# Performance work log

Measured on AMD Instinct MI355X. Metric: run time of the kernel, lower is better.

Reference implementation:

```python
import jax, jax.numpy as jnp
import numpy as np

N_P = 100000
N_A = 100000
IN = 128
H = 4
D = 32
E = 500000
ALPHA = 0.2


def _leaky(x, a=ALPHA):
    return jnp.where(x > 0, x, a * x)


def _gat_relation(Wh_src_rel, Wh_dst_self, a_src, a_dst, src, dst, n_dst):
    # Wh_src_rel: [Ns,H,D] relation-transformed source feats
    # Wh_dst_self: [Nd,H,D] self-transformed dest feats
    # a_src, a_dst: [H,D] attention vectors; src/dst: [E] edge index
    es = jnp.einsum('nhd,hd->nh', Wh_src_rel, a_src)  # [Ns,H]
    ed = jnp.einsum('nhd,hd->nh', Wh_dst_self, a_dst)  # [Nd,H]
    e = _leaky(es[src] + ed[dst])                      # [E,H]
    m = jax.ops.segment_max(e, dst, num_segments=n_dst)
    m = jnp.where(jnp.isfinite(m), m, 0.0)             # empty segments
    m = jax.lax.stop_gradient(m)
    ee = jnp.exp(e - m[dst])
    s = jax.ops.segment_sum(ee, dst, num_segments=n_dst)
    a = ee / s[dst]                                    # edge_softmax [E,H]
    msg = Wh_src_rel[src] * a[:, :, None]              # [E,H,D]
    return jax.ops.segment_sum(msg, dst, num_segments=n_dst)  # [Nd,H,D]


def setup_inputs() -> dict:
    key = jax.random.key(0)
    ks = jax.random.split(key, 32)
    inp = {
        'feat_P': jax.random.normal(ks[0], (N_P, IN), jnp.float32),
        'feat_A': jax.random.normal(ks[1], (N_A, IN), jnp.float32),
    }
    names = ['p2p', 'p2a', 'a2p', 'a2a']
    nsrc = {'p2p': N_P, 'p2a': N_P, 'a2p': N_A, 'a2a': N_A}
    ndst = {'p2p': N_P, 'p2a': N_A, 'a2p': N_P, 'a2a': N_A}
    for i, r in enumerate(names):
        inp['src_' + r] = jax.random.randint(ks[2 + 2 * i], (E,), 0, nsrc[r], jnp.int32)
        inp['dst_' + r] = jax.random.randint(ks[3 + 2 * i], (E,), 0, ndst[r], jnp.int32)
    # linear weights (torch Linear: y = x @ W.T + b); store as [IN, H*D]
    sc = 1.0 / np.sqrt(IN)
    for i, nm in enumerate(['P', 'A', 'p2p', 'p2a', 'a2p', 'a2a']):
        inp['W_' + nm] = jax.random.uniform(ks[10 + i], (IN, H * D), jnp.float32, -sc, sc)
        inp['b_' + nm] = jax.random.uniform(ks[16 + i], (H * D,), jnp.float32, -sc, sc)
    # attention vectors [H,D]
    for i, nm in enumerate(['p2p_src', 'p2p_dst', 'p2a_src', 'p2a_dst',
                            'a2p_src', 'a2p_dst', 'a2a_src', 'a2a_dst']):
        inp['att_' + nm] = jax.random.normal(ks[22 + i], (H, D), jnp.float32) * 0.1
    return inp


def reference(feat_P, feat_A,
              src_p2p, dst_p2p, src_p2a, dst_p2a,
              src_a2p, dst_a2p, src_a2a, dst_a2a,
              W_P, b_P, W_A, b_A, W_p2p, b_p2p, W_p2a, b_p2a,
              W_a2p, b_a2p, W_a2a, b_a2a,
              att_p2p_src, att_p2p_dst, att_p2a_src, att_p2a_dst,
              att_a2p_src, att_a2p_dst, att_a2a_src, att_a2a_dst):
    lin = lambda x, W, b: (x @ W + b).reshape(-1, H, D)
    Whp = lin(feat_P, W_P, b_P)      # [N_P,H,D]
    Wha = lin(feat_A, W_A, b_A)      # [N_A,H,D]
    Whp2p = lin(feat_P, W_p2p, b_p2p)
    Whp2a = lin(feat_P, W_p2a, b_p2a)
    Wha2p = lin(feat_A, W_a2p, b_a2p)
    Wha2a = lin(feat_A, W_a2a, b_a2a)
    ft_p2p = _gat_relation(Whp2p, Whp, att_p2p_src, att_p2p_dst, src_p2p, dst_p2p, N_P)
    ft_p2a = _gat_relation(Whp2a, Wha, att_p2a_src, att_p2a_dst, src_p2a, dst_p2a, N_A)
    ft_a2p = _gat_relation(Wha2p, Whp, att_a2p_src, att_a2p_dst, src_a2p, dst_a2p, N_P)
    ft_a2a = _gat_relation(Wha2a, Wha, att_a2a_src, att_a2a_dst, src_a2a, dst_a2a, N_A)
    h_P = jax.nn.relu(Whp + ft_p2p + ft_a2p)
    h_A = jax.nn.relu(Wha + ft_p2a + ft_a2a)
    return h_P, h_A
```

## Files before the change

### kernel.cpp

```cpp
#include <hip/hip_runtime.h>
#include <float.h>

#define ALPHA 0.2f
__device__ __forceinline__ float leakyf(float x) { return x > 0.0f ? x : ALPHA * x; }

__device__ __forceinline__ unsigned short f2bf(float f) {
    unsigned u = __float_as_uint(f);
    return (unsigned short)((u + 0x7FFFu + ((u >> 16) & 1u)) >> 16);
}
__device__ __forceinline__ float bflo(unsigned u) { return __uint_as_float(u << 16); }
__device__ __forceinline__ float bfhi(unsigned u) { return __uint_as_float(u & 0xFFFF0000u); }

typedef short bf16x8 __attribute__((ext_vector_type(8)));
typedef float f32x4 __attribute__((ext_vector_type(4)));

struct Ptr4i { const int* p0; const int* p1; const int* p2; const int* p3; };
struct PrepM { const float* W; const float* b; const float* attA; const float* attB; };

__global__ __launch_bounds__(256) void prep_kernel(
    PrepM m0, PrepM m1, PrepM m2, PrepM m3, PrepM m4, PrepM m5,
    bf16x8* __restrict__ wfrag, float* __restrict__ cd,
    int* __restrict__ bcnt, int nz)
{
    int mi = blockIdx.x;
    PrepM mm = (mi == 0) ? m0 : (mi == 1) ? m1 : (mi == 2) ? m2 :
               (mi == 3) ? m3 : (mi == 4) ? m4 : m5;
    int part = blockIdx.y;
    if (mi == 0 && part == 0) {
        for (int i = threadIdx.x; i < nz; i += 256) bcnt[i] = 0;
    }
    for (int ii = 0; ii < 3; ++ii) {
        int c = part * 576 + threadIdx.x + 256 * ii;
        if (c >= part * 576 + 576) continue;
        int t = c >> 8;
        int kstep = (c >> 6) & 3;
        int l = c & 63;
        int k0 = kstep * 32 + (l >> 4) * 8;
        bf16x8 out;
        if (t < 8) {
            int col = t * 16 + (l & 15);
            #pragma unroll
            for (int j = 0; j < 8; ++j)
                out[j] = (short)f2bf(mm.W[(size_t)(k0 + j) * 128 + col]);
        } else {
            int cl = l & 15;
            const float* att = nullptr; int h = 0;
            if (cl < 4 && mm.attA) { att = mm.attA; h = cl; }
            else if (cl >= 4 && cl < 8 && mm.attB) { att = mm.attB; h = cl - 4; }
            #pragma unroll
            for (int j = 0; j < 8; ++j) {
                float s = 0.f;
                if (att) {
                    const float* wrow = mm.W + (size_t)(k0 + j) * 128 + h * 32;
                    for (int d = 0; d < 32; ++d) s += wrow[d] * att[h * 32 + d];
                }
                out[j] = (short)f2bf(s);
            }
        }
        wfrag[(size_t)mi * 2304 + c] = out;
    }
    if (part == 0 && threadIdx.x < 8) {
        int cl = threadIdx.x;
        float s = 0.f;
        const float* att = nullptr; int h = 0;
        if (cl < 4 && mm.attA) { att = mm.attA; h = cl; }
        else if (cl >= 4 && mm.attB) { att = mm.attB; h = cl - 4; }
        if (att) for (int d = 0; d < 32; ++d) s += mm.b[h * 32 + d] * att[h * 32 + d];
        cd[mi * 8 + cl] = s;
    }
}

__device__ __forceinline__ void mfma_compute_store(
    const short* xs_s, const short* wl_s, int row0, int N,
    const float* __restrict__ b, float* __restrict__ o32, unsigned short* __restrict__ o16,
    float* __restrict__ dotA, float* __restrict__ dotB, const float* __restrict__ cd)
{
    int l = threadIdx.x & 63, w = threadIdx.x >> 6;
    int cl = l & 15, gq = l >> 4;
    f32x4 acc[9];
    #pragma unroll
    for (int t = 0; t < 9; ++t) acc[t] = (f32x4){0.f, 0.f, 0.f, 0.f};
    int arow = w * 16 + cl;
    #pragma unroll
    for (int ks = 0; ks < 4; ++ks) {
        int k8 = ks * 4 + gq;
        bf16x8 a = *(const bf16x8*)((const char*)xs_s + arow * 256 + ((k8 * 16) ^ ((arow & 7) << 4)));
        #pragma unroll
        for (int t = 0; t < 9; ++t) {
            bf16x8 bf = *(const bf16x8*)((const char*)wl_s + ((t * 4 + ks) * 64 + l) * 16);
            acc[t] = __builtin_amdgcn_mfma_f32_16x16x32_bf16(a, bf, acc[t], 0, 0, 0);
        }
    }
    int rbase = row0 + w * 16 + gq * 4;
    #pragma unroll
    for (int t = 0; t < 8; ++t) {
        int col = t * 16 + cl;
        float bias = b[col];
        #pragma unroll
        for (int j = 0; j < 4; ++j) {
            int row = rbase + j;
            if (row < N) {
                float v = acc[t][j] + bias;
                if (o32) o32[(size_t)row * 128 + col] = v;
                else     o16[(size_t)row * 128 + col] = f2bf(v);
            }
        }
    }
    if (cl < 8) {
        float cdv = cd[cl];
        float* dp = (cl < 4) ? dotA : dotB;
        int h = cl & 3;
        if (dp) {
            #pragma unroll
            for (int j = 0; j < 4; ++j) {
                int row = rbase + j;
                if (row < N) dp[(size_t)row * 4 + h] = acc[8][j] + cdv;
            }
        }
    }
}

struct Lin3Cfg {
    const float* x; int N; int blocks;
    const bf16x8* wfrag; const float* cd;
    const float* b0; float* o0; float* dA0; float* dB0;
    const float* b1; unsigned short* o1; float* dA1;
    const float* b2; unsigned short* o2; float* dA2;
};

__global__ __launch_bounds__(256) void lin3_mfma_kernel(Lin3Cfg cP, Lin3Cfg cA)
{
    __shared__ short xs_s[64 * 128];
    __shared__ short wl_s[2304 * 8];
    const bool isP = blockIdx.x < (unsigned)cP.blocks;
    const Lin3Cfg& c = isP ? cP : cA;
    const int bx = isP ? blockIdx.x : (blockIdx.x - cP.blocks);
    const int row0 = bx * 64;
    const int N = c.N;

    #pragma unroll
    for (int ii = 0; ii < 4; ++ii) {
        int ci = threadIdx.x + 256 * ii;
        int r = ci >> 4, k8 = ci & 15;
        int srcrow = row0 + r; if (srcrow >= N) srcrow = N - 1;
        const float4* gp = (const float4*)(c.x + (size_t)srcrow * 128 + k8 * 8);
        float4 v0 = gp[0], v1 = gp[1];
        bf16x8 p;
        p[0] = (short)f2bf(v0.x); p[1] = (short)f2bf(v0.y);
        p[2] = (short)f2bf(v0.z); p[3] = (short)f2bf(v0.w);
        p[4] = (short)f2bf(v1.x); p[5] = (short)f2bf(v1.y);
        p[6] = (short)f2bf(v1.z); p[7] = (short)f2bf(v1.w);
        *(bf16x8*)((char*)xs_s + r * 256 + ((k8 * 16) ^ ((r & 7) << 4))) = p;
    }
    #pragma unroll
    for (int ii = 0; ii < 9; ++ii)
        ((bf16x8*)wl_s)[threadIdx.x + 256 * ii] = c.wfrag[threadIdx.x + 256 * ii];
    __syncthreads();
    mfma_compute_store(xs_s, wl_s, row0, N, c.b0, c.o0, nullptr, c.dA0, c.dB0, c.cd);

    __syncthreads();
    #pragma unroll
    for (int ii = 0; ii < 9; ++ii)
        ((bf16x8*)wl_s)[threadIdx.x + 256 * ii] = c.wfrag[2304 + threadIdx.x + 256 * ii];
    __syncthreads();
    mfma_compute_store(xs_s, wl_s, row0, N, c.b1, nullptr, c.o1, c.dA1, nullptr, c.cd + 8);

    __syncthreads();
    #pragma unroll
    for (int ii = 0; ii < 9; ++ii)
        ((bf16x8*)wl_s)[threadIdx.x + 256 * ii] = c.wfrag[2 * 2304 + threadIdx.x + 256 * ii];
    __syncthreads();
    mfma_compute_store(xs_s, wl_s, row0, N, c.b2, nullptr, c.o2, c.dA2, nullptr, c.cd + 16);
}


__global__ __launch_bounds__(256) void binA_count_kernel(Ptr4i dsts, int* __restrict__ bcnt,
                                                         int nbkMax, int E)
{
    __shared__ int lh[4][128];
    ((int*)lh)[threadIdx.x] = 0;
    ((int*)lh)[threadIdx.x + 256] = 0;
    __syncthreads();
    int r = blockIdx.y;
    int w = threadIdx.x >> 6;
    const int* dst = (r == 0) ? dsts.p0 : (r == 1) ? dsts.p1 : (r == 2) ? dsts.p2 : dsts.p3;
    int base = blockIdx.x * 4096;
    #pragma unroll 4
    for (int ii = 0; ii < 16; ++ii) {
        int i = base + threadIdx.x + 256 * ii;
        if (i < E) atomicAdd(&lh[w][dst[i] >> 10], 1);
    }
    __syncthreads();
    if (threadIdx.x < 128) {
        int v = lh[0][threadIdx.x] + lh[1][threadIdx.x] + lh[2][threadIdx.x] + lh[3][threadIdx.x];
        if (v && threadIdx.x < nbkMax) atomicAdd(&bcnt[r * nbkMax + threadIdx.x], v);
    }
}

__global__ __launch_bounds__(512) void bin_scan_kernel(const int* __restrict__ bcnt,
                                                       int* __restrict__ bbase,
                                                       int* __restrict__ gwptr, int nbkMax)
{
    __shared__ int sh[4][128];
    int r = threadIdx.x >> 7, b = threadIdx.x & 127;
    int v = (b < nbkMax) ? bcnt[r * nbkMax + b] : 0;
    sh[r][b] = v;
    __syncthreads();
    #pragma unroll
    for (int off = 1; off < 128; off <<= 1) {
        int y = (b >= off) ? sh[r][b - off] : 0;
        __syncthreads();
        sh[r][b] += y;
        __syncthreads();
    }
    if (b < nbkMax) {
        int ex = sh[r][b] - v;
        bbase[r * nbkMax + b] = ex;
        gwptr[r * nbkMax + b] = ex;
    }
}

__global__ __launch_bounds__(256) void binA_scatter_kernel(Ptr4i dsts, Ptr4i srcs,
    int* __restrict__ gwptr, unsigned* __restrict__ packed, int nbkMax, int E)
{
    __shared__ int lh[128], loff[128], lptr[128], gb[128];
    __shared__ unsigned stg[4096];
    __shared__ unsigned short sb[4096];
    if (threadIdx.x < 128) lh[threadIdx.x] = 0;
    __syncthreads();
    int r = blockIdx.y;
    const int* dst = (r == 0) ? dsts.p0 : (r == 1) ? dsts.p1 : (r == 2) ? dsts.p2 : dsts.p3;
    const int* src = (r == 0) ? srcs.p0 : (r == 1) ? srcs.p1 : (r == 2) ? srcs.p2 : srcs.p3;
    int base = blockIdx.x * 4096;
    int d16[16], s16[16];
    #pragma unroll 4
    for (int ii = 0; ii < 16; ++ii) {
        int i = base + threadIdx.x + 256 * ii;
        if (i < E) {
            d16[ii] = dst[i];
            s16[ii] = src[i];
            atomicAdd(&lh[d16[ii] >> 10], 1);
        } else d16[ii] = -1;
    }
    __syncthreads();
    if (threadIdx.x == 0) {
        int run = 0;
        for (int b = 0; b < nbkMax; ++b) { loff[b] = run; lptr[b] = run; run += lh[b]; }
    }
    __syncthreads();
    #pragma unroll 4
    for (int ii = 0; ii < 16; ++ii) {
        if (d16[ii] >= 0) {
            int b = d16[ii] >> 10;
            int p = atomicAdd(&lptr[b], 1);
            stg[p] = ((unsigned)s16[ii] << 10) | (unsigned)(d16[ii] & 1023);
            sb[p] = (unsigned short)b;
        }
    }
    __syncthreads();
    if (threadIdx.x < nbkMax && lh[threadIdx.x])
        gb[threadIdx.x] = atomicAdd(&gwptr[r * nbkMax + threadIdx.x], lh[threadIdx.x]);
    __syncthreads();
    int tot = min(4096, E - base);
    #pragma unroll 4
    for (int ii = 0; ii < 16; ++ii) {
        int p = threadIdx.x + 256 * ii;
        if (p < tot) {
            int b = sb[p];
            packed[(size_t)r * E + gb[b] + (p - loff[b])] = stg[p];
        }
    }
}

__global__ __launch_bounds__(256) void binB_build_kernel(
    const unsigned* __restrict__ packed, const int* __restrict__ bcnt, const int* __restrict__ bbase,
    int nbkMax, int4 Ns, int E, int stride,
    int* __restrict__ start, int* __restrict__ deg, int* __restrict__ csrc)
{
    int r = blockIdx.y, b = blockIdx.x;
    int N = (r == 0) ? Ns.x : (r == 1) ? Ns.y : (r == 2) ? Ns.z : Ns.w;
    int dst0 = b << 10;
    if (dst0 >= N) return;
    int cnt  = bcnt[r * nbkMax + b];
    int base = bbase[r * nbkMax + b];
    __shared__ int hist[1024];
    __shared__ int sums[256];
    #pragma unroll
    for (int i = 0; i < 4; ++i) hist[threadIdx.x * 4 + i] = 0;
    __syncthreads();
    const unsigned* pk = packed + (size_t)r * E + base;
    for (int i = threadIdx.x; i < cnt; i += 256)
        atomicAdd(&hist[pk[i] & 1023], 1);
    __syncthreads();
    int v4[4], s = 0;
    #pragma unroll
    for (int i = 0; i < 4; ++i) { v4[i] = hist[threadIdx.x * 4 + i]; s += v4[i]; }
    sums[threadIdx.x] = s;
    __syncthreads();
    #pragma unroll
    for (int off = 1; off < 256; off <<= 1) {
        int y = (threadIdx.x >= off) ? sums[threadIdx.x - off] : 0;
        __syncthreads();
        sums[threadIdx.x] += y;
        __syncthreads();
    }
    int run = sums[threadIdx.x] - s;
    int* st = start + (size_t)r * stride;
    int* dg = deg   + (size_t)r * stride;
    #pragma unroll
    for (int i = 0; i < 4; ++i) {
        int idx = threadIdx.x * 4 + i;
        int d = dst0 + idx;
        if (d < N) { dg[d] = v4[i]; st[d] = base + run; }
        hist[idx] = run;
        run += v4[i];
    }
    __syncthreads();
    int* cs = csrc + (size_t)r * E + base;
    for (int i = threadIdx.x; i < cnt; i += 256) {
        unsigned e = pk[i];
        int p = atomicAdd(&hist[e & 1023], 1);
        cs[p] = (int)(e >> 10);
    }
}

struct GatRel {
    const int* start; const int* deg; const int* csrc;
    const unsigned short* Wh; const float* es; const float* ed;
};
struct GatCfg { float* out; int Nd; int blocks; GatRel rel0, rel1; };

__global__ __launch_bounds__(256) void gat_node_kernel(GatCfg cP, GatCfg cA)
{
    const bool isP = blockIdx.x < (unsigned)cP.blocks;
    const GatCfg& c = isP ? cP : cA;
    const int bx = isP ? blockIdx.x : (blockIdx.x - cP.blocks);
    int gid = bx * 256 + threadIdx.x;
    int d = gid >> 6;
    if (d >= c.Nd) return;
    int lane = threadIdx.x & 63;
    int q = lane >> 4;
    int l = lane & 15;
    int h = l >> 2;

    const float4* orow = (const float4*)(c.out + (size_t)d * 128);
    float4 A0 = orow[l * 2], A1 = orow[l * 2 + 1];

    #pragma unroll
    for (int rel = 0; rel < 2; ++rel) {
        const GatRel& R = rel ? c.rel1 : c.rel0;
        int st = R.start[d];
        int n  = R.deg[d];
        if (n == 0) continue;
        const uint4* W4 = (const uint4*)R.Wh;
        float edv = R.ed[(size_t)d * 4 + h];
        float sum = 0.f;
        float m0 = 0.f, m1 = 0.f, m2 = 0.f, m3 = 0.f;
        float m4 = 0.f, m5 = 0.f, m6 = 0.f, m7 = 0.f;
        int j = q;
        for (; j + 4 < n; j += 8) {
            int s0 = R.csrc[st + j];
            int s1 = R.csrc[st + j + 4];
            float p0 = __expf(leakyf(R.es[(size_t)s0 * 4 + h] + edv));
            float p1 = __expf(leakyf(R.es[(size_t)s1 * 4 + h] + edv));
            uint4 w0 = W4[(size_t)s0 * 16 + l];
            uint4 w1 = W4[(size_t)s1 * 16 + l];
            sum += p0 + p1;
            m0 += p0 * bflo(w0.x) + p1 * bflo(w1.x);
            m1 += p0 * bfhi(w0.x) + p1 * bfhi(w1.x);
            m2 += p0 * bflo(w0.y) + p1 * bflo(w1.y);
            m3 += p0 * bfhi(w0.y) + p1 * bfhi(w1.y);
            m4 += p0 * bflo(w0.z) + p1 * bflo(w1.z);
            m5 += p0 * bfhi(w0.z) + p1 * bfhi(w1.z);
            m6 += p0 * bflo(w0.w) + p1 * bflo(w1.w);
            m7 += p0 * bfhi(w0.w) + p1 * bfhi(w1.w);
        }
        if (j < n) {
            int s0 = R.csrc[st + j];
            float p0 = __expf(leakyf(R.es[(size_t)s0 * 4 + h] + edv));
            uint4 w0 = W4[(size_t)s0 * 16 + l];
            sum += p0;
            m0 += p0 * bflo(w0.x); m1 += p0 * bfhi(w0.x);
            m2 += p0 * bflo(w0.y); m3 += p0 * bfhi(w0.y);
            m4 += p0 * bflo(w0.z); m5 += p0 * bfhi(w0.z);
            m6 += p0 * bflo(w0.w); m7 += p0 * bfhi(w0.w);
        }
        #pragma unroll
        for (int off = 16; off < 64; off <<= 1) {
            sum += __shfl_xor(sum, off, 64);
            m0 += __shfl_xor(m0, off, 64); m1 += __shfl_xor(m1, off, 64);
            m2 += __shfl_xor(m2, off, 64); m3 += __shfl_xor(m3, off, 64);
            m4 += __shfl_xor(m4, off, 64); m5 += __shfl_xor(m5, off, 64);
            m6 += __shfl_xor(m6, off, 64); m7 += __shfl_xor(m7, off, 64);
        }
        float inv = 1.0f / sum;
        A0.x += m0 * inv; A0.y += m1 * inv; A0.z += m2 * inv; A0.w += m3 * inv;
        A1.x += m4 * inv; A1.y += m5 * inv; A1.z += m6 * inv; A1.w += m7 * inv;
    }
    if (lane < 16) {
        A0.x = fmaxf(A0.x, 0.f); A0.y = fmaxf(A0.y, 0.f);
        A0.z = fmaxf(A0.z, 0.f); A0.w = fmaxf(A0.w, 0.f);
        A1.x = fmaxf(A1.x, 0.f); A1.y = fmaxf(A1.y, 0.f);
        A1.z = fmaxf(A1.z, 0.f); A1.w = fmaxf(A1.w, 0.f);
        float4* ow = (float4*)(c.out + (size_t)d * 128);
        ow[l * 2] = A0; ow[l * 2 + 1] = A1;
    }
}

extern "C" void kernel_launch(void* const* d_in, const int* in_sizes, int n_in,
                              void* d_out, int out_size, void* d_ws, size_t ws_size,
                              hipStream_t stream)
{
    const float* feat_P = (const float*)d_in[0];
    const float* feat_A = (const float*)d_in[1];
    const int* src_p2p = (const int*)d_in[2];
    const int* dst_p2p = (const int*)d_in[3];
    const int* src_p2a = (const int*)d_in[4];
    const int* dst_p2a = (const int*)d_in[5];
    const int* src_a2p = (const int*)d_in[6];
    const int* dst_a2p = (const int*)d_in[7];
    const int* src_a2a = (const int*)d_in[8];
    const int* dst_a2a = (const int*)d_in[9];
    const float* W_P   = (const float*)d_in[10]; const float* b_P   = (const float*)d_in[11];
    const float* W_A   = (const float*)d_in[12]; const float* b_A   = (const float*)d_in[13];
    const float* W_p2p = (const float*)d_in[14]; const float* b_p2p = (const float*)d_in[15];
    const float* W_p2a = (const float*)d_in[16]; const float* b_p2a = (const float*)d_in[17];
    const float* W_a2p = (const float*)d_in[18]; const float* b_a2p = (const float*)d_in[19];
    const float* W_a2a = (const float*)d_in[20]; const float* b_a2a = (const float*)d_in[21];
    const float* att_p2p_src = (const float*)d_in[22];
    const float* att_p2p_dst = (const float*)d_in[23];
    const float* att_p2a_src = (const float*)d_in[24];
    const float* att_p2a_dst = (const float*)d_in[25];
    const float* att_a2p_src = (const float*)d_in[26];
    const float* att_a2p_dst = (const float*)d_in[27];
    const float* att_a2a_src = (const float*)d_in[28];
    const float* att_a2a_dst = (const float*)d_in[29];

    const int NP = in_sizes[0] / 128;
    const int NA = in_sizes[1] / 128;
    const int E  = in_sizes[2];
    const int stride = (NP > NA) ? NP : NA;
    const int nbkMax = (stride + 1023) >> 10;

    float* outP = (float*)d_out;
    float* outA = (float*)d_out + (size_t)NP * 128;

    char* ws = (char*)d_ws;
    size_t off = 0;
    auto alloc = [&](size_t bytes) -> void* {
        void* p = ws + off;
        off += (bytes + 255) & ~(size_t)255;
        return p;
    };
    unsigned short* Whp2p = (unsigned short*)alloc((size_t)NP * 128 * 2);
    unsigned short* Whp2a = (unsigned short*)alloc((size_t)NP * 128 * 2);
    unsigned short* Wha2p = (unsigned short*)alloc((size_t)NA * 128 * 2);
    unsigned short* Wha2a = (unsigned short*)alloc((size_t)NA * 128 * 2);
    float* es_p2p = (float*)alloc((size_t)NP * 16);
    float* es_p2a = (float*)alloc((size_t)NP * 16);
    float* es_a2p = (float*)alloc((size_t)NA * 16);
    float* es_a2a = (float*)alloc((size_t)NA * 16);
    float* ed_p2p = (float*)alloc((size_t)NP * 16);
    float* ed_a2p = (float*)alloc((size_t)NP * 16);
    float* ed_p2a = (float*)alloc((size_t)NA * 16);
    float* ed_a2a = (float*)alloc((size_t)NA * 16);
    int* deg    = (int*)alloc((size_t)4 * stride * 4);
    int* start  = (int*)alloc((size_t)4 * stride * 4);
    int* csrc   = (int*)alloc((size_t)4 * E * 4);
    unsigned* packed = (unsigned*)alloc((size_t)4 * E * 4);
    int* bcnt   = (int*)alloc((size_t)4 * nbkMax * 4);
    int* bbase  = (int*)alloc((size_t)4 * nbkMax * 4);
    int* gwptr  = (int*)alloc((size_t)4 * nbkMax * 4);
    bf16x8* wfrag = (bf16x8*)alloc((size_t)6 * 2304 * 16);
    float* cd     = (float*)alloc((size_t)6 * 8 * 4);

    Ptr4i dsts = {dst_p2p, dst_a2p, dst_p2a, dst_a2a};
    Ptr4i srcs = {src_p2p, src_a2p, src_p2a, src_a2a};
    int4 Ns = make_int4(NP, NP, NA, NA);

    {
        PrepM m0 = {W_P,   b_P,   att_p2p_dst, att_a2p_dst};
        PrepM m1 = {W_p2p, b_p2p, att_p2p_src, nullptr};
        PrepM m2 = {W_p2a, b_p2a, att_p2a_src, nullptr};
        PrepM m3 = {W_A,   b_A,   att_p2a_dst, att_a2a_dst};
        PrepM m4 = {W_a2p, b_a2p, att_a2p_src, nullptr};
        PrepM m5 = {W_a2a, b_a2a, att_a2a_src, nullptr};
        prep_kernel<<<dim3(6, 4), 256, 0, stream>>>(m0, m1, m2, m3, m4, m5, wfrag, cd,
                                                    bcnt, 4 * nbkMax);
    }

    {
        Lin3Cfg cP = {feat_P, NP, (NP + 63) / 64, wfrag, cd,
                      b_P, outP, ed_p2p, ed_a2p,
                      b_p2p, Whp2p, es_p2p,
                      b_p2a, Whp2a, es_p2a};
        Lin3Cfg cA = {feat_A, NA, (NA + 63) / 64, wfrag + (size_t)3 * 2304, cd + 24,
                      b_A, outA, ed_p2a, ed_a2a,
                      b_a2p, Wha2p, es_a2p,
                      b_a2a, Wha2a, es_a2a};
        lin3_mfma_kernel<<<cP.blocks + cA.blocks, 256, 0, stream>>>(cP, cA);
    }

    {
        dim3 gA((E + 4095) / 4096, 4);
        binA_count_kernel<<<gA, 256, 0, stream>>>(dsts, bcnt, nbkMax, E);
        bin_scan_kernel<<<1, 512, 0, stream>>>(bcnt, bbase, gwptr, nbkMax);
        binA_scatter_kernel<<<gA, 256, 0, stream>>>(dsts, srcs, gwptr, packed, nbkMax, E);
        binB_build_kernel<<<dim3(nbkMax, 4), 256, 0, stream>>>(packed, bcnt, bbase,
            nbkMax, Ns, E, stride, start, deg, csrc);
    }

    {
        GatCfg cP = {outP, NP, (NP * 64 + 255) / 256,
            {start + 0 * (size_t)stride, deg + 0 * (size_t)stride, csrc + 0 * (size_t)E, Whp2p, es_p2p, ed_p2p},
            {start + 1 * (size_t)stride, deg + 1 * (size_t)stride, csrc + 1 * (size_t)E, Wha2p, es_a2p, ed_a2p}};
        GatCfg cA = {outA, NA, (NA * 64 + 255) / 256,
            {start + 2 * (size_t)stride, deg + 2 * (size_t)stride, csrc + 2 * (size_t)E, Whp2a, es_p2a, ed_p2a},
            {start + 3 * (size_t)stride, deg + 3 * (size_t)stride, csrc + 3 * (size_t)E, Wha2a, es_a2a, ed_a2a}};
        gat_node_kernel<<<cP.blocks + cA.blocks, 256, 0, stream>>>(cP, cA);
    }
}
```

Baseline: 336.7 us.

## Merge edge binning stages into prep and linear kernels to cut launches

```diff
diff --git a/kernel.cpp b/kernel.cpp
--- a/kernel.cpp
+++ b/kernel.cpp
@@ -17,18 +17,37 @@
 struct Ptr4i { const int* p0; const int* p1; const int* p2; const int* p3; };
 struct PrepM { const float* W; const float* b; const float* attA; const float* attB; };
 
-__global__ __launch_bounds__(256) void prep_kernel(
+__global__ __launch_bounds__(256) void prep_count_kernel(
     PrepM m0, PrepM m1, PrepM m2, PrepM m3, PrepM m4, PrepM m5,
     bf16x8* __restrict__ wfrag, float* __restrict__ cd,
-    int* __restrict__ bcnt, int nz)
-{
-    int mi = blockIdx.x;
+    Ptr4i dsts, int* __restrict__ pcnt, int nblkE, int E, int nCount)
+{
+    __shared__ int lh[4][128];
+    if ((int)blockIdx.x < nCount) {
+        ((int*)lh)[threadIdx.x] = 0;
+        ((int*)lh)[threadIdx.x + 256] = 0;
+        __syncthreads();
+        int cb = blockIdx.x;
+        int r = cb & 3, bx = cb >> 2;
+        int w = threadIdx.x >> 6;
+        const int* dst = (r == 0) ? dsts.p0 : (r == 1) ? dsts.p1 : (r == 2) ? dsts.p2 : dsts.p3;
+        int base = bx * 4096;
+        #pragma unroll 4
+        for (int ii = 0; ii < 16; ++ii) {
+            int i = base + threadIdx.x + 256 * ii;
+            if (i < E) atomicAdd(&lh[w][dst[i] >> 10], 1);
+        }
+        __syncthreads();
+        if (threadIdx.x < 128)
+            pcnt[((size_t)r * nblkE + bx) * 128 + threadIdx.x] =
+                lh[0][threadIdx.x] + lh[1][threadIdx.x] + lh[2][threadIdx.x] + lh[3][threadIdx.x];
+        return;
+    }
+    int pb = blockIdx.x - nCount;
+    int mi = pb >> 2;
+    int part = pb & 3;
     PrepM mm = (mi == 0) ? m0 : (mi == 1) ? m1 : (mi == 2) ? m2 :
                (mi == 3) ? m3 : (mi == 4) ? m4 : m5;
-    int part = blockIdx.y;
-    if (mi == 0 && part == 0) {
-        for (int i = threadIdx.x; i < nz; i += 256) bcnt[i] = 0;
-    }
     for (int ii = 0; ii < 3; ++ii) {
         int c = part * 576 + threadIdx.x + 256 * ii;
         if (c >= part * 576 + 576) continue;
@@ -70,6 +89,33 @@
     }
 }
 
+__global__ __launch_bounds__(512) void scan_kernel(
+    const int* __restrict__ pcnt, int nblkE,
+    int* __restrict__ bcnt, int* __restrict__ bbase, int* __restrict__ gwptr, int nbkMax)
+{
+    __shared__ int sh[4][128];
+    int r = threadIdx.x >> 7, b = threadIdx.x & 127;
+    int v = 0;
+    if (b < nbkMax)
+        for (int i = 0; i < nblkE; ++i)
+            v += pcnt[((size_t)r * nblkE + i) * 128 + b];
+    sh[r][b] = v;
+    __syncthreads();
+    #pragma unroll
+    for (int off = 1; off < 128; off <<= 1) {
+        int y = (b >= off) ? sh[r][b - off] : 0;
+        __syncthreads();
+        sh[r][b] += y;
+        __syncthreads();
+    }
+    if (b < nbkMax) {
+        int ex = sh[r][b] - v;
+        bcnt[r * nbkMax + b]  = v;
+        bbase[r * nbkMax + b] = ex;
+        gwptr[r * nbkMax + b] = ex;
+    }
+}
+
 __device__ __forceinline__ void mfma_compute_store(
     const short* xs_s, const short* wl_s, int row0, int N,
     const float* __restrict__ b, float* __restrict__ o32, unsigned short* __restrict__ o16,
@@ -128,13 +174,71 @@
     const float* b2; unsigned short* o2; float* dA2;
 };
 
-__global__ __launch_bounds__(256) void lin3_mfma_kernel(Lin3Cfg cP, Lin3Cfg cA)
-{
-    __shared__ short xs_s[64 * 128];
-    __shared__ short wl_s[2304 * 8];
-    const bool isP = blockIdx.x < (unsigned)cP.blocks;
+__global__ __launch_bounds__(256) void lin3_scatter_kernel(
+    Lin3Cfg cP, Lin3Cfg cA, Ptr4i dsts, Ptr4i srcs,
+    int* __restrict__ gwptr, unsigned* __restrict__ packed, int nbkMax, int E, int nScat)
+{
+    __shared__ __align__(16) char smem[53248];
+    if ((int)blockIdx.x < nScat) {
+        int* lh   = (int*)smem;
+        int* loff = lh + 128;
+        int* lptr = lh + 256;
+        int* gb   = lh + 384;
+        unsigned* stg = (unsigned*)(smem + 2048);
+        unsigned short* sb = (unsigned short*)(smem + 2048 + 16384);
+        if (threadIdx.x < 128) lh[threadIdx.x] = 0;
+        __syncthreads();
+        int cb = blockIdx.x;
+        int r = cb & 3, bx = cb >> 2;
+        const int* dst = (r == 0) ? dsts.p0 : (r == 1) ? dsts.p1 : (r == 2) ? dsts.p2 : dsts.p3;
+        const int* src = (r == 0) ? srcs.p0 : (r == 1) ? srcs.p1 : (r == 2) ? srcs.p2 : srcs.p3;
+        int base = bx * 4096;
+        int d16[16], s16[16];
+        #pragma unroll 4
+        for (int ii = 0; ii < 16; ++ii) {
+            int i = base + threadIdx.x + 256 * ii;
+            if (i < E) {
+                d16[ii] = dst[i];
+                s16[ii] = src[i];
+                atomicAdd(&lh[d16[ii] >> 10], 1);
+            } else d16[ii] = -1;
+        }
+        __syncthreads();
+        if (threadIdx.x == 0) {
+            int run = 0;
+            for (int b = 0; b < nbkMax; ++b) { loff[b] = run; lptr[b] = run; run += lh[b]; }
+        }
+        __syncthreads();
+        #pragma unroll 4
+        for (int ii = 0; ii < 16; ++ii) {
+            if (d16[ii] >= 0) {
+                int b = d16[ii] >> 10;
+                int p = atomicAdd(&lptr[b], 1);
+                stg[p] = ((unsigned)s16[ii] << 10) | (unsigned)(d16[ii] & 1023);
+                sb[p] = (unsigned short)b;
+            }
+        }
+        __syncthreads();
+        if (threadIdx.x < nbkMax && lh[threadIdx.x])
+            gb[threadIdx.x] = atomicAdd(&gwptr[r * nbkMax + threadIdx.x], lh[threadIdx.x]);
+        __syncthreads();
+        int tot = min(4096, E - base);
+        #pragma unroll 4
+        for (int ii = 0; ii < 16; ++ii) {
+            int p = threadIdx.x + 256 * ii;
+            if (p < tot) {
+                int b = sb[p];
+                packed[(size_t)r * E + gb[b] + (p - loff[b])] = stg[p];
+            }
+        }
+        return;
+    }
+    short* xs_s = (short*)smem;
+    short* wl_s = (short*)(smem + 16384);
+    int bxl = blockIdx.x - nScat;
+    const bool isP = bxl < cP.blocks;
     const Lin3Cfg& c = isP ? cP : cA;
-    const int bx = isP ? blockIdx.x : (blockIdx.x - cP.blocks);
+    const int bx = isP ? bxl : (bxl - cP.blocks);
     const int row0 = bx * 64;
     const int N = c.N;
 
@@ -171,105 +275,6 @@
         ((bf16x8*)wl_s)[threadIdx.x + 256 * ii] = c.wfrag[2 * 2304 + threadIdx.x + 256 * ii];
     __syncthreads();
     mfma_compute_store(xs_s, wl_s, row0, N, c.b2, nullptr, c.o2, c.dA2, nullptr, c.cd + 16);
-}
-
-
-__global__ __launch_bounds__(256) void binA_count_kernel(Ptr4i dsts, int* __restrict__ bcnt,
-                                                         int nbkMax, int E)
-{
-    __shared__ int lh[4][128];
-    ((int*)lh)[threadIdx.x] = 0;
-    ((int*)lh)[threadIdx.x + 256] = 0;
-    __syncthreads();
-    int r = blockIdx.y;
-    int w = threadIdx.x >> 6;
-    const int* dst = (r == 0) ? dsts.p0 : (r == 1) ? dsts.p1 : (r == 2) ? dsts.p2 : dsts.p3;
-    int base = blockIdx.x * 4096;
-    #pragma unroll 4
-    for (int ii = 0; ii < 16; ++ii) {
-        int i = base + threadIdx.x + 256 * ii;
-        if (i < E) atomicAdd(&lh[w][dst[i] >> 10], 1);
-    }
-    __syncthreads();
-    if (threadIdx.x < 128) {
-        int v = lh[0][threadIdx.x] + lh[1][threadIdx.x] + lh[2][threadIdx.x] + lh[3][threadIdx.x];
-        if (v && threadIdx.x < nbkMax) atomicAdd(&bcnt[r * nbkMax + threadIdx.x], v);
-    }
-}
-
-__global__ __launch_bounds__(512) void bin_scan_kernel(const int* __restrict__ bcnt,
-                                                       int* __restrict__ bbase,
-                                                       int* __restrict__ gwptr, int nbkMax)
-{
-    __shared__ int sh[4][128];
-    int r = threadIdx.x >> 7, b = threadIdx.x & 127;
-    int v = (b < nbkMax) ? bcnt[r * nbkMax + b] : 0;
-    sh[r][b] = v;
-    __syncthreads();
-    #pragma unroll
-    for (int off = 1; off < 128; off <<= 1) {
-        int y = (b >= off) ? sh[r][b - off] : 0;
-        __syncthreads();
-        sh[r][b] += y;
-        __syncthreads();
-    }
-    if (b < nbkMax) {
-        int ex = sh[r][b] - v;
-        bbase[r * nbkMax + b] = ex;
-        gwptr[r * nbkMax + b] = ex;
-    }
-}
-
-__global__ __launch_bounds__(256) void binA_scatter_kernel(Ptr4i dsts, Ptr4i srcs,
-    int* __restrict__ gwptr, unsigned* __restrict__ packed, int nbkMax, int E)
-{
-    __shared__ int lh[128], loff[128], lptr[128], gb[128];
-    __shared__ unsigned stg[4096];
-    __shared__ unsigned short sb[4096];
-    if (threadIdx.x < 128) lh[threadIdx.x] = 0;
-    __syncthreads();
-    int r = blockIdx.y;
-    const int* dst = (r == 0) ? dsts.p0 : (r == 1) ? dsts.p1 : (r == 2) ? dsts.p2 : dsts.p3;
-    const int* src = (r == 0) ? srcs.p0 : (r == 1) ? srcs.p1 : (r == 2) ? srcs.p2 : srcs.p3;
-    int base = blockIdx.x * 4096;
-    int d16[16], s16[16];
-    #pragma unroll 4
-    for (int ii = 0; ii < 16; ++ii) {
-        int i = base + threadIdx.x + 256 * ii;
-        if (i < E) {
-            d16[ii] = dst[i];
-            s16[ii] = src[i];
-            atomicAdd(&lh[d16[ii] >> 10], 1);
-        } else d16[ii] = -1;
-    }
-    __syncthreads();
-    if (threadIdx.x == 0) {
-        int run = 0;
-        for (int b = 0; b < nbkMax; ++b) { loff[b] = run; lptr[b] = run; run += lh[b]; }
-    }
-    __syncthreads();
-    #pragma unroll 4
-    for (int ii = 0; ii < 16; ++ii) {
-        if (d16[ii] >= 0) {
-            int b = d16[ii] >> 10;
-            int p = atomicAdd(&lptr[b], 1);
-            stg[p] = ((unsigned)s16[ii] << 10) | (unsigned)(d16[ii] & 1023);
-            sb[p] = (unsigned short)b;
-        }
-    }
-    __syncthreads();
-    if (threadIdx.x < nbkMax && lh[threadIdx.x])
-        gb[threadIdx.x] = atomicAdd(&gwptr[r * nbkMax + threadIdx.x], lh[threadIdx.x]);
-    __syncthreads();
-    int tot = min(4096, E - base);
-    #pragma unroll 4
-    for (int ii = 0; ii < 16; ++ii) {
-        int p = threadIdx.x + 256 * ii;
-        if (p < tot) {
-            int b = sb[p];
-            packed[(size_t)r * E + gb[b] + (p - loff[b])] = stg[p];
-        }
-    }
 }
 
 __global__ __launch_bounds__(256) void binB_build_kernel(
@@ -441,6 +446,8 @@
     const int E  = in_sizes[2];
     const int stride = (NP > NA) ? NP : NA;
     const int nbkMax = (stride + 1023) >> 10;
+    const int nblkE  = (E + 4095) / 4096;
+    const int nCount = 4 * nblkE;
 
     float* outP = (float*)d_out;
     float* outA = (float*)d_out + (size_t)NP * 128;
@@ -471,6 +478,7 @@
     int* bcnt   = (int*)alloc((size_t)4 * nbkMax * 4);
     int* bbase  = (int*)alloc((size_t)4 * nbkMax * 4);
     int* gwptr  = (int*)alloc((size_t)4 * nbkMax * 4);
+    int* pcnt   = (int*)alloc((size_t)4 * nblkE * 128 * 4);
     bf16x8* wfrag = (bf16x8*)alloc((size_t)6 * 2304 * 16);
     float* cd     = (float*)alloc((size_t)6 * 8 * 4);
 
@@ -485,9 +493,11 @@
         PrepM m3 = {W_A,   b_A,   att_p2a_dst, att_a2a_dst};
         PrepM m4 = {W_a2p, b_a2p, att_a2p_src, nullptr};
         PrepM m5 = {W_a2a, b_a2a, att_a2a_src, nullptr};
-        prep_kernel<<<dim3(6, 4), 256, 0, stream>>>(m0, m1, m2, m3, m4, m5, wfrag, cd,
-                                                    bcnt, 4 * nbkMax);
-    }
+        prep_count_kernel<<<nCount + 24, 256, 0, stream>>>(m0, m1, m2, m3, m4, m5,
+            wfrag, cd, dsts, pcnt, nblkE, E, nCount);
+    }
+
+    scan_kernel<<<1, 512, 0, stream>>>(pcnt, nblkE, bcnt, bbase, gwptr, nbkMax);
 
     {
         Lin3Cfg cP = {feat_P, NP, (NP + 63) / 64, wfrag, cd,
@@ -498,17 +508,12 @@
                       b_A, outA, ed_p2a, ed_a2a,
                       b_a2p, Wha2p, es_a2p,
                       b_a2a, Wha2a, es_a2a};
-        lin3_mfma_kernel<<<cP.blocks + cA.blocks, 256, 0, stream>>>(cP, cA);
-    }
-
-    {
-        dim3 gA((E + 4095) / 4096, 4);
-        binA_count_kernel<<<gA, 256, 0, stream>>>(dsts, bcnt, nbkMax, E);
-        bin_scan_kernel<<<1, 512, 0, stream>>>(bcnt, bbase, gwptr, nbkMax);
-        binA_scatter_kernel<<<gA, 256, 0, stream>>>(dsts, srcs, gwptr, packed, nbkMax, E);
-        binB_build_kernel<<<dim3(nbkMax, 4), 256, 0, stream>>>(packed, bcnt, bbase,
-            nbkMax, Ns, E, stride, start, deg, csrc);
-    }
+        lin3_scatter_kernel<<<nCount + cP.blocks + cA.blocks, 256, 0, stream>>>(
+            cP, cA, dsts, srcs, gwptr, packed, nbkMax, E, nCount);
+    }
+
+    binB_build_kernel<<<dim3(nbkMax, 4), 256, 0, stream>>>(packed, bcnt, bbase,
+        nbkMax, Ns, E, stride, start, deg, csrc);
 
     {
         GatCfg cP = {outP, NP, (NP * 64 + 255) / 256,
```

Measured after the change: 333.9 us, median of 2. Within noise of the previous version (-0.8%).
